# Kernel tuning notes

Hardware: AMD Instinct MI355X
Metric: run time of the kernel (lower is better)

The kernel has to match this reference:

```python
import jax, jax.numpy as jnp
import numpy as np

B, E, K, U = 2048, 96, 8, 1024  # batch, word_emb_size, num_basis, num_units


def setup_inputs() -> dict:
    key = jax.random.key(0)
    k1, k2, k3, k4, k5 = jax.random.split(key, 5)
    inputs = jax.random.normal(k1, (B, E + K), dtype=jnp.float32)
    h_tm1 = jax.random.normal(k2, (B, U), dtype=jnp.float32)
    c_tm1 = jax.random.normal(k3, (B, U), dtype=jnp.float32)
    basis_kernel = jax.random.normal(k4, (E, K, 4 * U), dtype=jnp.float32) * 0.05
    basis_recurrent_kernel = jax.random.normal(k5, (U, K, 4 * U), dtype=jnp.float32) * 0.05
    bias = jnp.zeros((4 * U,), dtype=jnp.float32)
    return {
        "inputs": inputs,
        "h_tm1": h_tm1,
        "c_tm1": c_tm1,
        "basis_kernel": basis_kernel,
        "basis_recurrent_kernel": basis_recurrent_kernel,
        "bias": bias,
    }


def reference(inputs, h_tm1, c_tm1, basis_kernel, basis_recurrent_kernel, bias):
    word_emb_size = basis_kernel.shape[0]
    num_units = basis_recurrent_kernel.shape[0]
    x = inputs[:, :word_emb_size]           # [B, E]
    c_prob = inputs[:, word_emb_size:]      # [B, K]
    # Algebraically identical to composing a per-example kernel
    # (sum_k c_prob[b,k] * W[:,k,:]) and doing a per-example matmul:
    # z[b,z] = sum_e sum_k x[b,e] * c_prob[b,k] * W[e,k,z] (+ recurrent term).
    z = (jnp.einsum('be,ekz,bk->bz', x, basis_kernel, c_prob)
         + jnp.einsum('bu,ukz,bk->bz', h_tm1, basis_recurrent_kernel, c_prob)
         + bias)
    z0, z1, z2, z3 = jnp.split(z, 4, axis=1)  # each [B, U]
    i = jax.nn.sigmoid(z0)
    f = jax.nn.sigmoid(z1)
    c = f * c_tm1 + i * jnp.tanh(z2)
    o = jax.nn.sigmoid(z3)
    h = o * jnp.tanh(c)
    return (h, c)
```

## Files before the change

kernel.cpp:

```cpp
#include <hip/hip_runtime.h>
#include <stdint.h>
#include <stddef.h>

#define B_SZ   2048
#define E_SZ   96
#define K_SZ   8
#define U_SZ   1024
#define EK     (E_SZ * K_SZ)
#define KD     ((E_SZ + U_SZ) * K_SZ)
#define NZ     (4 * U_SZ)

typedef _Float16 f16_t;
typedef _Float16 f16x8 __attribute__((ext_vector_type(8)));
typedef float    f32x4  __attribute__((ext_vector_type(4)));
typedef float    f32x16 __attribute__((ext_vector_type(16)));

typedef __attribute__((address_space(3))) void       lds_void;
typedef const __attribute__((address_space(1))) void gbl_void;

__device__ __forceinline__ void gload16(const void* g, void* l) {
    __builtin_amdgcn_global_load_lds((gbl_void*)g, (lds_void*)l, 16, 0, 0);
}

__global__ __launch_bounds__(256) void build_a_kernel(
    const float* __restrict__ inputs,
    const float* __restrict__ h_tm1,
    f16_t* __restrict__ Ah)
{
    unsigned tid = blockIdx.x * 256u + threadIdx.x;
    unsigned b   = tid / 1120u;
    unsigned i8  = tid - b * 1120u;

    const float* row = inputs + (size_t)b * (E_SZ + K_SZ);
    f32x4 cp0 = *(const f32x4*)(row + E_SZ);
    f32x4 cp1 = *(const f32x4*)(row + E_SZ + 4);
    float cp[8] = {cp0[0], cp0[1], cp0[2], cp0[3], cp1[0], cp1[1], cp1[2], cp1[3]};

    float base = (i8 < (unsigned)E_SZ) ? row[i8]
                                       : h_tm1[(size_t)b * U_SZ + (i8 - E_SZ)];
    f16x8 hi;
    #pragma unroll
    for (int k = 0; k < 8; ++k)
        hi[k] = (f16_t)(base * cp[k]);
    *(f16x8*)(Ah + (size_t)b * KD + (size_t)i8 * 8) = hi;
}

__global__ __launch_bounds__(256) void transpose_w_kernel(
    const float* __restrict__ bk,
    const float* __restrict__ brk,
    f16_t* __restrict__ Wth)
{
    __shared__ float tile[64][65];
    int r0 = blockIdx.x * 64;
    int z0 = blockIdx.y * 64;
    const float* src = (r0 < EK) ? (bk + (size_t)r0 * NZ)
                                 : (brk + (size_t)(r0 - EK) * NZ);
    int t  = threadIdx.x;
    int rl = t >> 4;
    int c4 = (t & 15) * 4;

    #pragma unroll
    for (int i = 0; i < 4; ++i) {
        int r = rl + i * 16;
        f32x4 v = *(const f32x4*)(src + (size_t)r * NZ + z0 + c4);
        tile[r][c4 + 0] = v[0];
        tile[r][c4 + 1] = v[1];
        tile[r][c4 + 2] = v[2];
        tile[r][c4 + 3] = v[3];
    }
    __syncthreads();
    int zl = t >> 3;
    int c8 = (t & 7) * 8;
    #pragma unroll
    for (int i = 0; i < 2; ++i) {
        int z = zl + i * 32;
        f16x8 hi;
        #pragma unroll
        for (int j = 0; j < 8; ++j)
            hi[j] = (f16_t)tile[c8 + j][z];
        *(f16x8*)(Wth + (size_t)(z0 + z) * KD + r0 + c8) = hi;
    }
}

#define BM 256
#define BN 128
#define BK 32
#define NT 280
#define ABY (BM * BK * 2)
#define WBY (BN * BK * 2)
#define BUFB (ABY + WBY)
#define SMEM_BYTES 131072

__global__ __launch_bounds__(512, 2) void basis_lstm_gemm_kernel(
    const f16_t* __restrict__ Ah, const f16_t* __restrict__ Wth,
    const float* __restrict__ bias, const float* __restrict__ c_tm1,
    float* __restrict__ out)
{
    extern __shared__ __align__(16) char smem[];

    int id  = blockIdx.x;
    int v   = (id & 7) * 32 + (id >> 3);
    int bm0 = (v & 7) * BM;
    int jb0 = (v >> 3) * 32;

    int t    = threadIdx.x;
    int lane = t & 63;
    int w    = t >> 6;
    int wm   = w >> 1;
    int wn   = w & 1;
    int l31  = lane & 31;
    int lh   = lane >> 5;

    f32x16 acc[2][2];
    #pragma unroll
    for (int mi = 0; mi < 2; ++mi)
        #pragma unroll
        for (int ni = 0; ni < 2; ++ni)
            #pragma unroll
            for (int e = 0; e < 16; ++e)
                acc[mi][ni][e] = 0.f;

    auto stageA = [&](int kt) {
        char* buf = smem + (kt & 3) * BUFB;
        int   ko  = kt * BK;
        #pragma unroll
        for (int i = 0; i < 2; ++i) {
            int q = i * 512 + t;
            int row = q >> 2, cc = q & 3;
            size_t off = (size_t)(bm0 + row) * KD + ko + ((cc ^ ((row ^ (row >> 2)) & 3)) << 3);
            gload16(Ah + off, buf + q * 16);
        }
    };
    auto stageB = [&](int kt) {
        char* buf = smem + (kt & 3) * BUFB + ABY;
        int   ko  = kt * BK;
        int q = t, c = q >> 2, cc = q & 3;
        int z = ((c >> 5) << 10) + jb0 + (c & 31);
        size_t off = (size_t)z * KD + ko + ((cc ^ ((c ^ (c >> 2)) & 3)) << 3);
        gload16(Wth + off, buf + q * 16);
    };

    auto phase = [&](int kt, int ks, int stg) {
        const char* buf = smem + (kt & 3) * BUFB;
        f16x8 af[2], wf[2];
        #pragma unroll
        for (int mi = 0; mi < 2; ++mi) {
            int r  = wm * 64 + mi * 32 + l31;
            int sc = (ks * 2 + lh) ^ ((r ^ (r >> 2)) & 3);
            af[mi] = *(const f16x8*)(buf + r * 64 + sc * 16);
        }
        #pragma unroll
        for (int ni = 0; ni < 2; ++ni) {
            int r  = wn * 64 + ni * 32 + l31;
            int sc = (ks * 2 + lh) ^ ((r ^ (r >> 2)) & 3);
            wf[ni] = *(const f16x8*)(buf + ABY + r * 64 + sc * 16);
        }
        if (stg == 1) stageA(kt + 3);
        else if (stg == 2) stageB(kt + 3);
        __builtin_amdgcn_s_barrier();
        __builtin_amdgcn_s_setprio(1);
        #pragma unroll
        for (int mi = 0; mi < 2; ++mi)
            #pragma unroll
            for (int ni = 0; ni < 2; ++ni)
                acc[mi][ni] = __builtin_amdgcn_mfma_f32_32x32x16_f16(af[mi], wf[ni], acc[mi][ni], 0, 0, 0);
        __builtin_amdgcn_s_setprio(0);
    };

    stageA(0); stageB(0);
    stageA(1); stageB(1);
    stageA(2); stageB(2);
    asm volatile("s_waitcnt vmcnt(6)" ::: "memory");
    __builtin_amdgcn_s_barrier();

    for (int kt = 0; kt < NT - 3; ++kt) {
        phase(kt, 0, 1);
        __builtin_amdgcn_s_barrier();
        phase(kt, 1, 2);
        asm volatile("s_waitcnt vmcnt(6)" ::: "memory");
        __builtin_amdgcn_s_barrier();
    }
    phase(NT - 3, 0, 0); __builtin_amdgcn_s_barrier();
    phase(NT - 3, 1, 0);
    asm volatile("s_waitcnt vmcnt(3)" ::: "memory");
    __builtin_amdgcn_s_barrier();
    phase(NT - 2, 0, 0); __builtin_amdgcn_s_barrier();
    phase(NT - 2, 1, 0);
    asm volatile("s_waitcnt vmcnt(0)" ::: "memory");
    __builtin_amdgcn_s_barrier();
    phase(NT - 1, 0, 0); __builtin_amdgcn_s_barrier();
    phase(NT - 1, 1, 0);
    __syncthreads();

    float* zb = (float*)smem;
    #pragma unroll
    for (int mi = 0; mi < 2; ++mi)
        #pragma unroll
        for (int ni = 0; ni < 2; ++ni)
            #pragma unroll
            for (int r = 0; r < 16; ++r) {
                int row = wm * 64 + mi * 32 + (r & 3) + 8 * (r >> 2) + 4 * lh;
                int col = wn * 64 + ni * 32 + l31;
                zb[row * 128 + col] = acc[mi][ni][r];
            }
    __syncthreads();

    int jj = t & 31;
    int rg = t >> 5;
    int jg = jb0 + jj;
    float b0 = bias[jg];
    float b1 = bias[U_SZ + jg];
    float b2 = bias[2 * U_SZ + jg];
    float b3 = bias[3 * U_SZ + jg];
    float* out_h = out;
    float* out_c = out + (size_t)B_SZ * U_SZ;
    #pragma unroll
    for (int i = 0; i < 16; ++i) {
        int   row = rg * 16 + i;
        int   br  = bm0 + row;
        float zi = zb[row * 128 +  0 + jj] + b0;
        float zf = zb[row * 128 + 32 + jj] + b1;
        float zc = zb[row * 128 + 64 + jj] + b2;
        float zo = zb[row * 128 + 96 + jj] + b3;
        float ig = 1.f / (1.f + __expf(-zi));
        float fg = 1.f / (1.f + __expf(-zf));
        float og = 1.f / (1.f + __expf(-zo));
        float cn = fg * c_tm1[(size_t)br * U_SZ + jg] + ig * tanhf(zc);
        float hn = og * tanhf(cn);
        out_h[(size_t)br * U_SZ + jg] = hn;
        out_c[(size_t)br * U_SZ + jg] = cn;
    }
}

extern "C" void kernel_launch(void* const* d_in, const int* in_sizes, int n_in,
                              void* d_out, int out_size, void* d_ws, size_t ws_size,
                              hipStream_t stream) {
    const float* inputs = (const float*)d_in[0];
    const float* h_tm1  = (const float*)d_in[1];
    const float* c_tm1  = (const float*)d_in[2];
    const float* bk     = (const float*)d_in[3];
    const float* brk    = (const float*)d_in[4];
    const float* bias   = (const float*)d_in[5];

    char*  ws  = (char*)d_ws;
    f16_t* Ah  = (f16_t*)(ws);
    f16_t* Wth = (f16_t*)(ws + 36700160u);

    hipFuncSetAttribute((const void*)basis_lstm_gemm_kernel,
                        hipFuncAttributeMaxDynamicSharedMemorySize, SMEM_BYTES);

    hipLaunchKernelGGL(build_a_kernel, dim3(8960), dim3(256), 0, stream,
                       inputs, h_tm1, Ah);
    hipLaunchKernelGGL(transpose_w_kernel, dim3(140, 64), dim3(256), 0, stream,
                       bk, brk, Wth);
    hipLaunchKernelGGL(basis_lstm_gemm_kernel, dim3(256), dim3(512), SMEM_BYTES, stream,
                       Ah, Wth, bias, c_tm1, (float*)d_out);
}
```

Measured before the change: 421.8 us.

## Use 256x256 GEMM tiles with split-K and a separate LSTM reduce kernel

Each GEMM block now computes a 256x256 output tile instead of 256x128, which doubles arithmetic per loaded byte. To keep 256 blocks, the K dimension is split into two halves. Partial z sums go to a workspace buffer, and a new kernel adds the two halves, applies the bias and the LSTM gates. The pipeline also collapses to one barrier per k-tile. In exchange it writes and reads about 64 MB of fp32 partials, uses 128 KB of LDS with larger per-block register accumulators that may limit occupancy, and adds a kernel launch.

```diff
diff --git a/kernel.cpp b/kernel.cpp
--- a/kernel.cpp
+++ b/kernel.cpp
@@ -83,46 +83,50 @@
 }
 
 #define BM 256
-#define BN 128
+#define BN 256
 #define BK 32
-#define NT 280
+#define KHALF 4480
+#define NT 140
 #define ABY (BM * BK * 2)
 #define WBY (BN * BK * 2)
 #define BUFB (ABY + WBY)
-#define SMEM_BYTES 131072
+#define SMEM_BYTES (4 * BUFB)
 
 __global__ __launch_bounds__(512, 2) void basis_lstm_gemm_kernel(
     const f16_t* __restrict__ Ah, const f16_t* __restrict__ Wth,
-    const float* __restrict__ bias, const float* __restrict__ c_tm1,
-    float* __restrict__ out)
+    float* __restrict__ zpart)
 {
     extern __shared__ __align__(16) char smem[];
 
-    int id  = blockIdx.x;
-    int v   = (id & 7) * 32 + (id >> 3);
-    int bm0 = (v & 7) * BM;
-    int jb0 = (v >> 3) * 32;
+    int id   = blockIdx.x;
+    int xcd  = id & 7;
+    int rest = id >> 3;
+    int kh   = rest & 1;
+    int bm0  = ((rest >> 1) & 7) * BM;
+    int jb   = xcd * 2 + (rest >> 4);
+    int kbase = kh * KHALF;
+    float* zp = zpart + (size_t)kh * B_SZ * NZ;
 
     int t    = threadIdx.x;
     int lane = t & 63;
     int w    = t >> 6;
-    int wm   = w >> 1;
-    int wn   = w & 1;
+    int wm   = w & 1;
+    int wn   = w >> 1;
     int l31  = lane & 31;
     int lh   = lane >> 5;
 
-    f32x16 acc[2][2];
-    #pragma unroll
-    for (int mi = 0; mi < 2; ++mi)
+    f32x16 acc[4][2];
+    #pragma unroll
+    for (int mi = 0; mi < 4; ++mi)
         #pragma unroll
         for (int ni = 0; ni < 2; ++ni)
             #pragma unroll
             for (int e = 0; e < 16; ++e)
                 acc[mi][ni][e] = 0.f;
 
-    auto stageA = [&](int kt) {
+    auto stage = [&](int kt) {
         char* buf = smem + (kt & 3) * BUFB;
-        int   ko  = kt * BK;
+        int   ko  = kbase + kt * BK;
         #pragma unroll
         for (int i = 0; i < 2; ++i) {
             int q = i * 512 + t;
@@ -130,106 +134,104 @@
             size_t off = (size_t)(bm0 + row) * KD + ko + ((cc ^ ((row ^ (row >> 2)) & 3)) << 3);
             gload16(Ah + off, buf + q * 16);
         }
+        #pragma unroll
+        for (int i = 0; i < 2; ++i) {
+            int q = i * 512 + t;
+            int c = q >> 2, cc = q & 3;
+            int z = ((c >> 6) << 10) + jb * 64 + (c & 63);
+            size_t off = (size_t)z * KD + ko + ((cc ^ ((c ^ (c >> 2)) & 3)) << 3);
+            gload16(Wth + off, buf + ABY + q * 16);
+        }
     };
-    auto stageB = [&](int kt) {
-        char* buf = smem + (kt & 3) * BUFB + ABY;
-        int   ko  = kt * BK;
-        int q = t, c = q >> 2, cc = q & 3;
-        int z = ((c >> 5) << 10) + jb0 + (c & 31);
-        size_t off = (size_t)z * KD + ko + ((cc ^ ((c ^ (c >> 2)) & 3)) << 3);
-        gload16(Wth + off, buf + q * 16);
-    };
-
-    auto phase = [&](int kt, int ks, int stg) {
-        const char* buf = smem + (kt & 3) * BUFB;
-        f16x8 af[2], wf[2];
-        #pragma unroll
-        for (int mi = 0; mi < 2; ++mi) {
-            int r  = wm * 64 + mi * 32 + l31;
+
+    auto cslice = [&](const char* buf, int ks) {
+        f16x8 af[4], wf[2];
+        #pragma unroll
+        for (int mi = 0; mi < 4; ++mi) {
+            int r  = wm * 128 + mi * 32 + l31;
             int sc = (ks * 2 + lh) ^ ((r ^ (r >> 2)) & 3);
             af[mi] = *(const f16x8*)(buf + r * 64 + sc * 16);
         }
         #pragma unroll
         for (int ni = 0; ni < 2; ++ni) {
-            int r  = wn * 64 + ni * 32 + l31;
-            int sc = (ks * 2 + lh) ^ ((r ^ (r >> 2)) & 3);
-            wf[ni] = *(const f16x8*)(buf + ABY + r * 64 + sc * 16);
-        }
-        if (stg == 1) stageA(kt + 3);
-        else if (stg == 2) stageB(kt + 3);
-        __builtin_amdgcn_s_barrier();
+            int c  = wn * 64 + ni * 32 + l31;
+            int sc = (ks * 2 + lh) ^ ((c ^ (c >> 2)) & 3);
+            wf[ni] = *(const f16x8*)(buf + ABY + c * 64 + sc * 16);
+        }
         __builtin_amdgcn_s_setprio(1);
         #pragma unroll
-        for (int mi = 0; mi < 2; ++mi)
+        for (int mi = 0; mi < 4; ++mi)
             #pragma unroll
             for (int ni = 0; ni < 2; ++ni)
                 acc[mi][ni] = __builtin_amdgcn_mfma_f32_32x32x16_f16(af[mi], wf[ni], acc[mi][ni], 0, 0, 0);
         __builtin_amdgcn_s_setprio(0);
     };
 
-    stageA(0); stageB(0);
-    stageA(1); stageB(1);
-    stageA(2); stageB(2);
-    asm volatile("s_waitcnt vmcnt(6)" ::: "memory");
+    stage(0); stage(1); stage(2);
+    asm volatile("s_waitcnt vmcnt(8)" ::: "memory");
     __builtin_amdgcn_s_barrier();
 
-    for (int kt = 0; kt < NT - 3; ++kt) {
-        phase(kt, 0, 1);
-        __builtin_amdgcn_s_barrier();
-        phase(kt, 1, 2);
-        asm volatile("s_waitcnt vmcnt(6)" ::: "memory");
-        __builtin_amdgcn_s_barrier();
-    }
-    phase(NT - 3, 0, 0); __builtin_amdgcn_s_barrier();
-    phase(NT - 3, 1, 0);
-    asm volatile("s_waitcnt vmcnt(3)" ::: "memory");
-    __builtin_amdgcn_s_barrier();
-    phase(NT - 2, 0, 0); __builtin_amdgcn_s_barrier();
-    phase(NT - 2, 1, 0);
-    asm volatile("s_waitcnt vmcnt(0)" ::: "memory");
-    __builtin_amdgcn_s_barrier();
-    phase(NT - 1, 0, 0); __builtin_amdgcn_s_barrier();
-    phase(NT - 1, 1, 0);
-    __syncthreads();
-
-    float* zb = (float*)smem;
-    #pragma unroll
-    for (int mi = 0; mi < 2; ++mi)
-        #pragma unroll
-        for (int ni = 0; ni < 2; ++ni)
+    #pragma unroll 1
+    for (int kt = 0; kt < NT; ++kt) {
+        if (kt + 3 < NT) stage(kt + 3);
+        const char* buf = smem + (kt & 3) * BUFB;
+        cslice(buf, 0);
+        cslice(buf, 1);
+        if (kt <= NT - 4) {
+            asm volatile("s_waitcnt vmcnt(8)" ::: "memory");
+        } else if (kt == NT - 3) {
+            asm volatile("s_waitcnt vmcnt(4)" ::: "memory");
+        } else if (kt == NT - 2) {
+            asm volatile("s_waitcnt vmcnt(0)" ::: "memory");
+        }
+        if (kt < NT - 1) __builtin_amdgcn_s_barrier();
+    }
+
+    #pragma unroll
+    for (int ni = 0; ni < 2; ++ni) {
+        int c    = wn * 64 + ni * 32 + l31;
+        int zcol = ((c >> 6) << 10) + jb * 64 + (c & 63);
+        #pragma unroll
+        for (int mi = 0; mi < 4; ++mi) {
             #pragma unroll
             for (int r = 0; r < 16; ++r) {
-                int row = wm * 64 + mi * 32 + (r & 3) + 8 * (r >> 2) + 4 * lh;
-                int col = wn * 64 + ni * 32 + l31;
-                zb[row * 128 + col] = acc[mi][ni][r];
+                int row = wm * 128 + mi * 32 + (r & 3) + 8 * (r >> 2) + 4 * lh;
+                zp[(size_t)(bm0 + row) * NZ + zcol] = acc[mi][ni][r];
             }
-    __syncthreads();
-
-    int jj = t & 31;
-    int rg = t >> 5;
-    int jg = jb0 + jj;
-    float b0 = bias[jg];
-    float b1 = bias[U_SZ + jg];
-    float b2 = bias[2 * U_SZ + jg];
-    float b3 = bias[3 * U_SZ + jg];
-    float* out_h = out;
-    float* out_c = out + (size_t)B_SZ * U_SZ;
-    #pragma unroll
-    for (int i = 0; i < 16; ++i) {
-        int   row = rg * 16 + i;
-        int   br  = bm0 + row;
-        float zi = zb[row * 128 +  0 + jj] + b0;
-        float zf = zb[row * 128 + 32 + jj] + b1;
-        float zc = zb[row * 128 + 64 + jj] + b2;
-        float zo = zb[row * 128 + 96 + jj] + b3;
-        float ig = 1.f / (1.f + __expf(-zi));
-        float fg = 1.f / (1.f + __expf(-zf));
-        float og = 1.f / (1.f + __expf(-zo));
-        float cn = fg * c_tm1[(size_t)br * U_SZ + jg] + ig * tanhf(zc);
-        float hn = og * tanhf(cn);
-        out_h[(size_t)br * U_SZ + jg] = hn;
-        out_c[(size_t)br * U_SZ + jg] = cn;
-    }
+        }
+    }
+}
+
+__global__ __launch_bounds__(256) void lstm_reduce_kernel(
+    const float* __restrict__ zpart, const float* __restrict__ bias,
+    const float* __restrict__ c_tm1, float* __restrict__ out)
+{
+    int b  = blockIdx.x;
+    int j4 = threadIdx.x * 4;
+    const float* zp0 = zpart + (size_t)b * NZ;
+    const float* zp1 = zpart + (size_t)B_SZ * NZ + (size_t)b * NZ;
+
+    f32x4 zg[4];
+    #pragma unroll
+    for (int g = 0; g < 4; ++g) {
+        f32x4 a = *(const f32x4*)(zp0 + g * U_SZ + j4);
+        f32x4 c = *(const f32x4*)(zp1 + g * U_SZ + j4);
+        f32x4 bb = *(const f32x4*)(bias + g * U_SZ + j4);
+        zg[g] = a + c + bb;
+    }
+    f32x4 cprev = *(const f32x4*)(c_tm1 + (size_t)b * U_SZ + j4);
+    f32x4 ho, co;
+    #pragma unroll
+    for (int e = 0; e < 4; ++e) {
+        float ig = 1.f / (1.f + __expf(-zg[0][e]));
+        float fg = 1.f / (1.f + __expf(-zg[1][e]));
+        float og = 1.f / (1.f + __expf(-zg[3][e]));
+        float cn = fg * cprev[e] + ig * tanhf(zg[2][e]);
+        co[e] = cn;
+        ho[e] = og * tanhf(cn);
+    }
+    *(f32x4*)(out + (size_t)b * U_SZ + j4) = ho;
+    *(f32x4*)(out + (size_t)B_SZ * U_SZ + (size_t)b * U_SZ + j4) = co;
 }
 
 extern "C" void kernel_launch(void* const* d_in, const int* in_sizes, int n_in,
@@ -242,9 +244,10 @@
     const float* brk    = (const float*)d_in[4];
     const float* bias   = (const float*)d_in[5];
 
-    char*  ws  = (char*)d_ws;
-    f16_t* Ah  = (f16_t*)(ws);
-    f16_t* Wth = (f16_t*)(ws + 36700160u);
+    char*  ws    = (char*)d_ws;
+    f16_t* Ah    = (f16_t*)(ws);
+    f16_t* Wth   = (f16_t*)(ws + 36700160u);
+    float* zpart = (float*)(ws + 36700160u + 73400320u);
 
     hipFuncSetAttribute((const void*)basis_lstm_gemm_kernel,
                         hipFuncAttributeMaxDynamicSharedMemorySize, SMEM_BYTES);
@@ -254,5 +257,7 @@
     hipLaunchKernelGGL(transpose_w_kernel, dim3(140, 64), dim3(256), 0, stream,
                        bk, brk, Wth);
     hipLaunchKernelGGL(basis_lstm_gemm_kernel, dim3(256), dim3(512), SMEM_BYTES, stream,
-                       Ah, Wth, bias, c_tm1, (float*)d_out);
-}
+                       Ah, Wth, zpart);
+    hipLaunchKernelGGL(lstm_reduce_kernel, dim3(B_SZ), dim3(256), 0, stream,
+                       zpart, bias, c_tm1, (float*)d_out);
+}
```

After: 418.1 us. Within noise of the previous version (-0.9%).
